# Kernel optimization log

Measured on AMD Instinct MI355X. Metric: run time of the kernel, lower is better.

## Reference

```python
import jax, jax.numpy as jnp
import numpy as np

DIM = 256
WIN = 7
HEADS = 8
HEAD_DIM = DIM // HEADS
N = WIN * WIN
NW = 64          # windows per image (56x56 map / 7x7 windows)
BATCH = 2048     # num_windows * image_batch (64 * 32)
SCALE = HEAD_DIM ** -0.5


def _relative_position_index(win_h, win_w):
    coords = np.stack(np.meshgrid(np.arange(win_h), np.arange(win_w), indexing='ij'))  # (2, h, w)
    flat = coords.reshape(2, -1)                     # (2, N)
    rel = flat[:, :, None] - flat[:, None, :]        # (2, N, N)
    rel = rel.transpose(1, 2, 0).astype(np.int32)    # (N, N, 2)
    rel[:, :, 0] += win_h - 1
    rel[:, :, 1] += win_w - 1
    rel[:, :, 0] *= 2 * win_w - 1
    return jnp.asarray(rel.sum(-1))                  # (N, N) int32


def setup_inputs() -> dict:
    key = jax.random.key(0)
    ks = jax.random.split(key, 6)
    x = jax.random.normal(ks[0], (BATCH, N, DIM), dtype=jnp.float32)
    mask = jnp.zeros((NW, N, N), dtype=jnp.float32)  # shift mask (0 / -inf); zeros = no shift
    qkv_w = jax.random.normal(ks[1], (3 * DIM, DIM), dtype=jnp.float32) * 0.02
    qkv_b = jnp.zeros((3 * DIM,), dtype=jnp.float32)
    bias_table = jax.random.normal(ks[2], ((2 * WIN - 1) ** 2, HEADS), dtype=jnp.float32) * 0.02
    proj_w = jax.random.normal(ks[3], (DIM, DIM), dtype=jnp.float32) * 0.02
    proj_b = jnp.zeros((DIM,), dtype=jnp.float32)
    rel_index = _relative_position_index(WIN, WIN)
    return {"x": x, "mask": mask, "qkv_w": qkv_w, "qkv_b": qkv_b,
            "bias_table": bias_table, "proj_w": proj_w, "proj_b": proj_b,
            "rel_index": rel_index}


def reference(x, mask, qkv_w, qkv_b, bias_table, proj_w, proj_b, rel_index):
    B, n, C = x.shape
    qkv = x @ qkv_w.T + qkv_b                                  # (B, N, 3C)
    qkv = qkv.reshape(B, n, 3, HEADS, HEAD_DIM)
    qkv = jnp.transpose(qkv, (2, 0, 3, 1, 4))                  # (3, B, H, N, hd)
    q, k, v = qkv[0], qkv[1], qkv[2]
    attn = jnp.einsum('bhnd,bhmd->bhnm', q * SCALE, k)         # (B, H, N, N)
    rel_bias = bias_table[rel_index.reshape(-1)].reshape(n, n, HEADS)
    attn = attn + jnp.transpose(rel_bias, (2, 0, 1))[None]     # + (1, H, N, N)
    nW = mask.shape[0]
    attn = attn.reshape(B // nW, nW, HEADS, n, n) + mask[None, :, None]
    attn = attn.reshape(B, HEADS, n, n)
    attn = jax.nn.softmax(attn, axis=-1)
    out = jnp.einsum('bhnm,bhmd->bhnd', attn, v)               # (B, H, N, hd)
    out = jnp.transpose(out, (0, 2, 1, 3)).reshape(B, n, C)
    return out @ proj_w.T + proj_b
```

## Files before the change

kernel.cpp:

```cpp
#include <hip/hip_runtime.h>

typedef float f32x4 __attribute__((ext_vector_type(4)));
typedef short s16x8 __attribute__((ext_vector_type(8)));
typedef unsigned int u32x4 __attribute__((ext_vector_type(4)));
typedef unsigned int u32x2 __attribute__((ext_vector_type(2)));
typedef __bf16 bf16x2 __attribute__((ext_vector_type(2)));
typedef unsigned short u16;
typedef unsigned int u32;

#define QK_SCALE 0.17677669529663687f
#define LOG2E    1.4426950408889634f
#define QK_SCALE_L2E 0.25504614517377436f

__device__ __forceinline__ u16 f2bf(float f) {
    __bf16 b = (__bf16)f;
    return __builtin_bit_cast(u16, b);
}
__device__ __forceinline__ u32 pk2(float lo, float hi) {
    bf16x2 v;
    v[0] = (__bf16)lo;
    v[1] = (__bf16)hi;
    return __builtin_bit_cast(u32, v);
}
__device__ __forceinline__ float swap32(float v, bool lt32) {
    u32 xi = __builtin_bit_cast(u32, v);
    u32x2 r = __builtin_amdgcn_permlane32_swap(xi, xi, false, false);
    return __builtin_bit_cast(float, lt32 ? r[1] : r[0]);
}
__device__ __forceinline__ float swap16(float v, bool lo16) {
    u32 xi = __builtin_bit_cast(u32, v);
    u32x2 r = __builtin_amdgcn_permlane16_swap(xi, xi, false, false);
    return __builtin_bit_cast(float, lo16 ? r[1] : r[0]);
}

__device__ __forceinline__ s16x8 frag4(u32 r0u0, u32 r1u0, u32 r0u1, u32 r1u1,
                                       int aA, int aB, bool lo) {
    u32x4 w;
    u32 a, bq;
    a  = (u32)__builtin_amdgcn_ds_bpermute(aA, (int)r0u0);
    bq = (u32)__builtin_amdgcn_ds_bpermute(aA, (int)r0u1);
    w[0] = lo ? a : bq;
    a  = (u32)__builtin_amdgcn_ds_bpermute(aA, (int)r1u0);
    bq = (u32)__builtin_amdgcn_ds_bpermute(aA, (int)r1u1);
    w[1] = lo ? a : bq;
    a  = (u32)__builtin_amdgcn_ds_bpermute(aB, (int)r0u0);
    bq = (u32)__builtin_amdgcn_ds_bpermute(aB, (int)r0u1);
    w[2] = lo ? a : bq;
    a  = (u32)__builtin_amdgcn_ds_bpermute(aB, (int)r1u0);
    bq = (u32)__builtin_amdgcn_ds_bpermute(aB, (int)r1u1);
    w[3] = lo ? a : bq;
    return __builtin_bit_cast(s16x8, w);
}

#define WS_PROJW 393216
#define WS_BMC   524288
#define WS_F32_NEED (524288 + 8388608)

__global__ void prep(const float* __restrict__ qkv_w, const float* __restrict__ proj_w,
                     const float* __restrict__ bias_table, const int* __restrict__ rel_index,
                     const float* __restrict__ mask,
                     u16* __restrict__ wqkvC2, u16* __restrict__ projwC,
                     u16* __restrict__ bmC2, float* __restrict__ bmF, int use_f32) {
    int i = blockIdx.x * 256 + threadIdx.x;
    if (i < 196608) {
        int e = i & 7, lane = (i >> 3) & 63, ks = (i >> 9) & 7, dt = (i >> 12) & 1;
        int i2 = i >> 13, t = i2 % 3, h = i2 / 3;
        int c = lane & 15, g = lane >> 4;
        wqkvC2[i] = f2bf(qkv_w[(t * 256 + h * 32 + dt * 16 + c) * 256 + ks * 32 + g * 8 + e]);
    }
    if (i < 65536) {
        int e = i & 7, lane = (i >> 3) & 63, ks = (i >> 9) & 7, nt = (i >> 12) & 15;
        int c = lane & 15, g = lane >> 4;
        projwC[i] = f2bf(proj_w[(nt * 16 + c) * 256 + ks * 32 + g * 8 + e]);
    }
    {
        int j = i & 3, lane = (i >> 2) & 63, mtK = (i >> 8) & 3, ntQ = (i >> 10) & 3;
        int h = (i >> 12) & 7, wi = i >> 15;
        int c = lane & 15, g = lane >> 4;
        int q = ntQ * 16 + c, k = mtK * 16 + g * 4 + j;
        float v;
        if (k < 49) v = (q < 49) ? bias_table[rel_index[q * 49 + k] * 8 + h]
                                   + mask[wi * 2401 + q * 49 + k]
                                 : 0.f;
        else        v = -1e30f;
        v *= LOG2E;
        if (use_f32) bmF[i] = v;
        else         bmC2[i] = f2bf(v);
    }
}

#define OUTSB 22152
template<bool F32BM>
__global__ __launch_bounds__(256, 2)
void swin_attn(const float* __restrict__ x,
               const float* __restrict__ qkv_b,
               const float* __restrict__ proj_b,
               const u16* __restrict__ wqkvC2,
               const u16* __restrict__ projwC,
               const u16* __restrict__ bmC2,
               const float* __restrict__ bmF,
               float* __restrict__ out) {
    __shared__ __align__(16) u16 sm[35088];
    const int b = blockIdx.x, tid = threadIdx.x;
    const int wv = tid >> 6, lane = tid & 63, g = lane >> 4, c = lane & 15;
    const int wi = b & 63;
    const int VTb = 12936 + wv * 2304;
    const float* xw = x + (size_t)b * 12544;

    for (int i = tid; i < 49 * 64; i += 256) {
        int row = i >> 6, q4 = i & 63;
        float4 v = ((const float4*)xw)[i];
        uint2 s;
        s.x = pk2(v.x, v.y);
        s.y = pk2(v.z, v.w);
        *(uint2*)&sm[row * 264 + q4 * 4] = s;
    }
    __syncthreads();

    const int addrA = ((lane & 15) + ((lane & 16) << 1)) << 2;
    const int addrB = addrA + 64;
    const bool lo = lane < 32;
    const bool l16 = (lane & 16) == 0;
    const s16x8 zfrag = {0, 0, 0, 0, 0, 0, 0, 0};

#pragma unroll
    for (int hl = 0; hl < 2; ++hl) {
        const int h = wv * 2 + hl;

        f32x4 acc[6][4];
#pragma unroll
        for (int f = 0; f < 6; ++f)
#pragma unroll
            for (int tt = 0; tt < 4; ++tt) acc[f][tt] = f32x4{0.f, 0.f, 0.f, 0.f};

        s16x8 wf[2][6];
#pragma unroll
        for (int f = 0; f < 6; ++f)
            wf[0][f] = *(const s16x8*)&wqkvC2[(((h * 6 + f) * 8 + 0) * 64 + lane) * 8];
        s16x8 Xf[2][4];
#pragma unroll
        for (int tt = 0; tt < 4; ++tt)
            Xf[0][tt] = *(const s16x8*)&sm[(tt * 16 + c) * 264 + g * 8];
        if (c > 0) Xf[0][3] = zfrag;
#pragma unroll
        for (int ks = 0; ks < 8; ++ks) {
            if (ks < 7) {
#pragma unroll
                for (int f = 0; f < 6; ++f)
                    wf[(ks + 1) & 1][f] =
                        *(const s16x8*)&wqkvC2[(((h * 6 + f) * 8 + (ks + 1)) * 64 + lane) * 8];
#pragma unroll
                for (int tt = 0; tt < 4; ++tt)
                    Xf[(ks + 1) & 1][tt] = *(const s16x8*)&sm[(tt * 16 + c) * 264 + (ks + 1) * 32 + g * 8];
                if (c > 0) Xf[(ks + 1) & 1][3] = zfrag;
            }
            __builtin_amdgcn_s_setprio(1);
#pragma unroll
            for (int f = 0; f < 6; ++f)
#pragma unroll
                for (int tt = 0; tt < 4; ++tt)
                    acc[f][tt] = __builtin_amdgcn_mfma_f32_16x16x32_bf16(wf[ks & 1][f], Xf[ks & 1][tt], acc[f][tt], 0, 0, 0);
            __builtin_amdgcn_s_setprio(0);
        }

        u32 qp[4][2][2], kp[4][2][2];
#pragma unroll
        for (int f = 0; f < 6; ++f) {
            int t = f >> 1, dt = f & 1;
            f32x4 bv = *(const f32x4*)&qkv_b[t * 256 + h * 32 + dt * 16 + g * 4];
#pragma unroll
            for (int tt = 0; tt < 4; ++tt) {
                float v0 = acc[f][tt][0] + bv[0];
                float v1 = acc[f][tt][1] + bv[1];
                float v2 = acc[f][tt][2] + bv[2];
                float v3 = acc[f][tt][3] + bv[3];
                if (t == 0) {
                    qp[tt][dt][0] = pk2(v0 * QK_SCALE_L2E, v1 * QK_SCALE_L2E);
                    qp[tt][dt][1] = pk2(v2 * QK_SCALE_L2E, v3 * QK_SCALE_L2E);
                } else if (t == 1) {
                    kp[tt][dt][0] = pk2(v0, v1);
                    kp[tt][dt][1] = pk2(v2, v3);
                } else {
                    sm[VTb + (dt * 16 + g * 4 + 0) * 72 + tt * 16 + c] = f2bf(v0);
                    sm[VTb + (dt * 16 + g * 4 + 1) * 72 + tt * 16 + c] = f2bf(v1);
                    sm[VTb + (dt * 16 + g * 4 + 2) * 72 + tt * 16 + c] = f2bf(v2);
                    sm[VTb + (dt * 16 + g * 4 + 3) * 72 + tt * 16 + c] = f2bf(v3);
                }
            }
        }

        f32x4 bmf[4][4];
        u32 bm0[4][4], bm1[4][4];
        if constexpr (F32BM) {
#pragma unroll
            for (int ntQ = 0; ntQ < 4; ++ntQ)
#pragma unroll
                for (int mtK = 0; mtK < 4; ++mtK)
                    bmf[ntQ][mtK] = *(const f32x4*)&bmF[((((wi * 8 + h) * 4 + ntQ) * 4 + mtK) * 64 + lane) * 4];
        } else {
#pragma unroll
            for (int ntQ = 0; ntQ < 4; ++ntQ)
#pragma unroll
                for (int mtK = 0; mtK < 4; ++mtK) {
                    const u32* bp = (const u32*)&bmC2[((((wi * 8 + h) * 4 + ntQ) * 4 + mtK) * 64 + lane) * 4];
                    bm0[ntQ][mtK] = bp[0];
                    bm1[ntQ][mtK] = bp[1];
                }
        }

        s16x8 Qf[4], Kf[4];
#pragma unroll
        for (int nt = 0; nt < 4; ++nt)
            Qf[nt] = frag4(qp[nt][0][0], qp[nt][0][1], qp[nt][1][0], qp[nt][1][1], addrA, addrB, lo);
#pragma unroll
        for (int mt = 0; mt < 4; ++mt)
            Kf[mt] = frag4(kp[mt][0][0], kp[mt][0][1], kp[mt][1][0], kp[mt][1][1], addrA, addrB, lo);

#pragma unroll
        for (int ntQ = 0; ntQ < 4; ++ntQ) {
            f32x4 lvc[4];
            __builtin_amdgcn_s_setprio(1);
#pragma unroll
            for (int mtK = 0; mtK < 4; ++mtK) {
                if constexpr (F32BM) {
                    lvc[mtK] = __builtin_amdgcn_mfma_f32_16x16x32_bf16(Kf[mtK], Qf[ntQ], bmf[ntQ][mtK], 0, 0, 0);
                } else {
                    f32x4 z = {0.f, 0.f, 0.f, 0.f};
                    lvc[mtK] = __builtin_amdgcn_mfma_f32_16x16x32_bf16(Kf[mtK], Qf[ntQ], z, 0, 0, 0);
                }
            }
            __builtin_amdgcn_s_setprio(0);
            float m = -1e30f;
#pragma unroll
            for (int mtK = 0; mtK < 3; ++mtK) {
                if constexpr (!F32BM) {
                    u32 w0 = bm0[ntQ][mtK], w1 = bm1[ntQ][mtK];
                    lvc[mtK][0] += __builtin_bit_cast(float, w0 << 16);
                    lvc[mtK][1] += __builtin_bit_cast(float, w0 & 0xffff0000u);
                    lvc[mtK][2] += __builtin_bit_cast(float, w1 << 16);
                    lvc[mtK][3] += __builtin_bit_cast(float, w1 & 0xffff0000u);
                }
                m = fmaxf(m, fmaxf(fmaxf(lvc[mtK][0], lvc[mtK][1]),
                                   fmaxf(lvc[mtK][2], lvc[mtK][3])));
            }
            if constexpr (!F32BM)
                lvc[3][0] += __builtin_bit_cast(float, bm0[ntQ][3] << 16);
            m = fmaxf(m, lvc[3][0]);
            m = fmaxf(m, swap16(m, l16));
            m = fmaxf(m, swap32(m, lo));
            float s = 0.f;
#pragma unroll
            for (int mtK = 0; mtK < 3; ++mtK)
#pragma unroll
                for (int j = 0; j < 4; ++j) {
                    float e = __builtin_amdgcn_exp2f(lvc[mtK][j] - m);
                    lvc[mtK][j] = e;
                    s += e;
                }
            float e3 = __builtin_amdgcn_exp2f(lvc[3][0] - m);
            lvc[3][0] = e3;
            s += e3;
            s += swap16(s, l16);
            s += swap32(s, lo);
            float is = __builtin_amdgcn_rcpf(s);
            u32 ppc[4][2];
#pragma unroll
            for (int mtK = 0; mtK < 3; ++mtK) {
                ppc[mtK][0] = pk2(lvc[mtK][0] * is, lvc[mtK][1] * is);
                ppc[mtK][1] = pk2(lvc[mtK][2] * is, lvc[mtK][3] * is);
            }
            ppc[3][0] = pk2(lvc[3][0] * is, 0.f);
            ppc[3][1] = 0;

            f32x4 o[2] = {{0.f, 0.f, 0.f, 0.f}, {0.f, 0.f, 0.f, 0.f}};
#pragma unroll
            for (int ks2 = 0; ks2 < 2; ++ks2) {
                s16x8 Pf = frag4(ppc[2 * ks2][0], ppc[2 * ks2][1],
                                 ppc[2 * ks2 + 1][0], ppc[2 * ks2 + 1][1], addrA, addrB, lo);
                s16x8 Vf0 = *(const s16x8*)&sm[VTb + (0 * 16 + c) * 72 + ks2 * 32 + g * 8];
                s16x8 Vf1 = *(const s16x8*)&sm[VTb + (1 * 16 + c) * 72 + ks2 * 32 + g * 8];
                __builtin_amdgcn_s_setprio(1);
                o[0] = __builtin_amdgcn_mfma_f32_16x16x32_bf16(Pf, Vf0, o[0], 0, 0, 0);
                o[1] = __builtin_amdgcn_mfma_f32_16x16x32_bf16(Pf, Vf1, o[1], 0, 0, 0);
                __builtin_amdgcn_s_setprio(0);
            }
#pragma unroll
            for (int ndt = 0; ndt < 2; ++ndt) {
                int colb = (wv * 2 + hl) * 32 + ndt * 16 + c;
                int row = ntQ * 16 + g * 4;
                if (row < 49)     sm[OUTSB + row * 264 + colb] = f2bf(o[ndt][0]);
                if (row + 1 < 49) sm[OUTSB + (row + 1) * 264 + colb] = f2bf(o[ndt][1]);
                if (row + 2 < 49) sm[OUTSB + (row + 2) * 264 + colb] = f2bf(o[ndt][2]);
                if (row + 3 < 49) sm[OUTSB + (row + 3) * 264 + colb] = f2bf(o[ndt][3]);
            }
        }
    }

    s16x8 pf[2][4];
#pragma unroll
    for (int n = 0; n < 4; ++n)
        pf[0][n] = *(const s16x8*)&projwC[(((wv * 4 + n) * 8 + 0) * 64 + lane) * 8];
    __syncthreads();

    f32x4 pacc[4][4];
#pragma unroll
    for (int mt = 0; mt < 4; ++mt)
#pragma unroll
        for (int n = 0; n < 4; ++n) pacc[mt][n] = f32x4{0.f, 0.f, 0.f, 0.f};
#pragma unroll
    for (int ks = 0; ks < 8; ++ks) {
        if (ks < 7) {
#pragma unroll
            for (int n = 0; n < 4; ++n)
                pf[(ks + 1) & 1][n] =
                    *(const s16x8*)&projwC[(((wv * 4 + n) * 8 + (ks + 1)) * 64 + lane) * 8];
        }
        s16x8 ao[4];
#pragma unroll
        for (int mt = 0; mt < 4; ++mt) {
            int row = mt * 16 + c; row = row > 48 ? 48 : row;
            ao[mt] = *(const s16x8*)&sm[OUTSB + row * 264 + ks * 32 + g * 8];
        }
        __builtin_amdgcn_s_setprio(1);
#pragma unroll
        for (int n = 0; n < 4; ++n)
#pragma unroll
            for (int mt = 0; mt < 4; ++mt)
                pacc[mt][n] = __builtin_amdgcn_mfma_f32_16x16x32_bf16(ao[mt], pf[ks & 1][n], pacc[mt][n], 0, 0, 0);
        __builtin_amdgcn_s_setprio(0);
    }
    float* ob = out + (size_t)b * 12544;
#pragma unroll
    for (int n = 0; n < 4; ++n) {
        int col = (wv * 4 + n) * 16 + c;
        float pb = proj_b[col];
#pragma unroll
        for (int mt = 0; mt < 4; ++mt)
#pragma unroll
            for (int j = 0; j < 4; ++j) {
                int row = mt * 16 + g * 4 + j;
                if (row < 49) ob[row * 256 + col] = pacc[mt][n][j] + pb;
            }
    }
}

extern "C" void kernel_launch(void* const* d_in, const int* in_sizes, int n_in,
                              void* d_out, int out_size, void* d_ws, size_t ws_size,
                              hipStream_t stream) {
    const float* x          = (const float*)d_in[0];
    const float* mask       = (const float*)d_in[1];
    const float* qkv_w      = (const float*)d_in[2];
    const float* qkv_b      = (const float*)d_in[3];
    const float* bias_table = (const float*)d_in[4];
    const float* proj_w     = (const float*)d_in[5];
    const float* proj_b     = (const float*)d_in[6];
    const int*   rel_index  = (const int*)d_in[7];

    u16*   wqkvC2 = (u16*)d_ws;
    u16*   projwC = (u16*)((char*)d_ws + WS_PROJW);
    u16*   bmC2   = (u16*)((char*)d_ws + WS_BMC);
    float* bmF    = (float*)((char*)d_ws + WS_BMC);

    const bool f32bm = ws_size >= (size_t)WS_F32_NEED;

    prep<<<8192, 256, 0, stream>>>(qkv_w, proj_w, bias_table, rel_index, mask,
                                   wqkvC2, projwC, bmC2, bmF, (int)f32bm);
    if (f32bm)
        swin_attn<true><<<2048, 256, 0, stream>>>(x, qkv_b, proj_b, wqkvC2, projwC,
                                                  bmC2, bmF, (float*)d_out);
    else
        swin_attn<false><<<2048, 256, 0, stream>>>(x, qkv_b, proj_b, wqkvC2, projwC,
                                                   bmC2, bmF, (float*)d_out);
}
```

Before: 106.8 us.

## Stage Q/K/P/V fragments through LDS instead of ds_bpermute shuffles

```diff
diff --git a/kernel.cpp b/kernel.cpp
--- a/kernel.cpp
+++ b/kernel.cpp
@@ -2,13 +2,11 @@
 
 typedef float f32x4 __attribute__((ext_vector_type(4)));
 typedef short s16x8 __attribute__((ext_vector_type(8)));
-typedef unsigned int u32x4 __attribute__((ext_vector_type(4)));
 typedef unsigned int u32x2 __attribute__((ext_vector_type(2)));
 typedef __bf16 bf16x2 __attribute__((ext_vector_type(2)));
 typedef unsigned short u16;
 typedef unsigned int u32;
 
-#define QK_SCALE 0.17677669529663687f
 #define LOG2E    1.4426950408889634f
 #define QK_SCALE_L2E 0.25504614517377436f
 
@@ -31,25 +29,6 @@
     u32 xi = __builtin_bit_cast(u32, v);
     u32x2 r = __builtin_amdgcn_permlane16_swap(xi, xi, false, false);
     return __builtin_bit_cast(float, lo16 ? r[1] : r[0]);
-}
-
-__device__ __forceinline__ s16x8 frag4(u32 r0u0, u32 r1u0, u32 r0u1, u32 r1u1,
-                                       int aA, int aB, bool lo) {
-    u32x4 w;
-    u32 a, bq;
-    a  = (u32)__builtin_amdgcn_ds_bpermute(aA, (int)r0u0);
-    bq = (u32)__builtin_amdgcn_ds_bpermute(aA, (int)r0u1);
-    w[0] = lo ? a : bq;
-    a  = (u32)__builtin_amdgcn_ds_bpermute(aA, (int)r1u0);
-    bq = (u32)__builtin_amdgcn_ds_bpermute(aA, (int)r1u1);
-    w[1] = lo ? a : bq;
-    a  = (u32)__builtin_amdgcn_ds_bpermute(aB, (int)r0u0);
-    bq = (u32)__builtin_amdgcn_ds_bpermute(aB, (int)r0u1);
-    w[2] = lo ? a : bq;
-    a  = (u32)__builtin_amdgcn_ds_bpermute(aB, (int)r1u0);
-    bq = (u32)__builtin_amdgcn_ds_bpermute(aB, (int)r1u1);
-    w[3] = lo ? a : bq;
-    return __builtin_bit_cast(s16x8, w);
 }
 
 #define WS_PROJW 393216
@@ -89,7 +68,6 @@
     }
 }
 
-#define OUTSB 22152
 template<bool F32BM>
 __global__ __launch_bounds__(256, 2)
 void swin_attn(const float* __restrict__ x,
@@ -100,29 +78,29 @@
                const u16* __restrict__ bmC2,
                const float* __restrict__ bmF,
                float* __restrict__ out) {
-    __shared__ __align__(16) u16 sm[35088];
+    __shared__ __align__(16) u16 sm[38152];
     const int b = blockIdx.x, tid = threadIdx.x;
     const int wv = tid >> 6, lane = tid & 63, g = lane >> 4, c = lane & 15;
     const int wi = b & 63;
-    const int VTb = 12936 + wv * 2304;
+    const int WB = 12936 + wv * 6304;
     const float* xw = x + (size_t)b * 12544;
 
     for (int i = tid; i < 49 * 64; i += 256) {
         int row = i >> 6, q4 = i & 63;
         float4 v = ((const float4*)xw)[i];
-        uint2 s;
-        s.x = pk2(v.x, v.y);
-        s.y = pk2(v.z, v.w);
-        *(uint2*)&sm[row * 264 + q4 * 4] = s;
+        u32x2 s;
+        s[0] = pk2(v.x, v.y);
+        s[1] = pk2(v.z, v.w);
+        *(u32x2*)&sm[row * 264 + q4 * 4] = s;
     }
     __syncthreads();
 
-    const int addrA = ((lane & 15) + ((lane & 16) << 1)) << 2;
-    const int addrB = addrA + 64;
     const bool lo = lane < 32;
     const bool l16 = (lane & 16) == 0;
     const s16x8 zfrag = {0, 0, 0, 0, 0, 0, 0, 0};
 
+    u32 opk[2][4][2][2];
+
 #pragma unroll
     for (int hl = 0; hl < 2; ++hl) {
         const int h = wv * 2 + hl;
@@ -158,72 +136,85 @@
 #pragma unroll
             for (int f = 0; f < 6; ++f)
 #pragma unroll
-                for (int tt = 0; tt < 4; ++tt)
-                    acc[f][tt] = __builtin_amdgcn_mfma_f32_16x16x32_bf16(wf[ks & 1][f], Xf[ks & 1][tt], acc[f][tt], 0, 0, 0);
+                for (int tt = 0; tt < 4; ++tt) {
+                    if (f < 4)
+                        acc[f][tt] = __builtin_amdgcn_mfma_f32_16x16x32_bf16(wf[ks & 1][f], Xf[ks & 1][tt], acc[f][tt], 0, 0, 0);
+                    else
+                        acc[f][tt] = __builtin_amdgcn_mfma_f32_16x16x32_bf16(Xf[ks & 1][tt], wf[ks & 1][f], acc[f][tt], 0, 0, 0);
+                }
             __builtin_amdgcn_s_setprio(0);
         }
 
-        u32 qp[4][2][2], kp[4][2][2];
 #pragma unroll
         for (int f = 0; f < 6; ++f) {
             int t = f >> 1, dt = f & 1;
-            f32x4 bv = *(const f32x4*)&qkv_b[t * 256 + h * 32 + dt * 16 + g * 4];
-#pragma unroll
-            for (int tt = 0; tt < 4; ++tt) {
-                float v0 = acc[f][tt][0] + bv[0];
-                float v1 = acc[f][tt][1] + bv[1];
-                float v2 = acc[f][tt][2] + bv[2];
-                float v3 = acc[f][tt][3] + bv[3];
-                if (t == 0) {
-                    qp[tt][dt][0] = pk2(v0 * QK_SCALE_L2E, v1 * QK_SCALE_L2E);
-                    qp[tt][dt][1] = pk2(v2 * QK_SCALE_L2E, v3 * QK_SCALE_L2E);
-                } else if (t == 1) {
-                    kp[tt][dt][0] = pk2(v0, v1);
-                    kp[tt][dt][1] = pk2(v2, v3);
-                } else {
-                    sm[VTb + (dt * 16 + g * 4 + 0) * 72 + tt * 16 + c] = f2bf(v0);
-                    sm[VTb + (dt * 16 + g * 4 + 1) * 72 + tt * 16 + c] = f2bf(v1);
-                    sm[VTb + (dt * 16 + g * 4 + 2) * 72 + tt * 16 + c] = f2bf(v2);
-                    sm[VTb + (dt * 16 + g * 4 + 3) * 72 + tt * 16 + c] = f2bf(v3);
-                }
-            }
-        }
-
-        f32x4 bmf[4][4];
-        u32 bm0[4][4], bm1[4][4];
-        if constexpr (F32BM) {
-#pragma unroll
-            for (int ntQ = 0; ntQ < 4; ++ntQ)
+            if (t < 2) {
+                f32x4 bv = *(const f32x4*)&qkv_b[t * 256 + h * 32 + dt * 16 + g * 4];
+                int base = (t == 0) ? WB : WB + 2000;
+#pragma unroll
+                for (int tt = 0; tt < 4; ++tt) {
+                    int row = tt * 16 + c;
+                    float v0 = acc[f][tt][0] + bv[0];
+                    float v1 = acc[f][tt][1] + bv[1];
+                    float v2 = acc[f][tt][2] + bv[2];
+                    float v3 = acc[f][tt][3] + bv[3];
+                    if (t == 0) {
+                        v0 *= QK_SCALE_L2E; v1 *= QK_SCALE_L2E;
+                        v2 *= QK_SCALE_L2E; v3 *= QK_SCALE_L2E;
+                    }
+                    if (row < 50) {
+                        u32x2 s;
+                        s[0] = pk2(v0, v1);
+                        s[1] = pk2(v2, v3);
+                        *(u32x2*)&sm[base + row * 40 + dt * 16 + g * 4] = s;
+                    }
+                }
+            } else {
+                float bvs = qkv_b[512 + h * 32 + dt * 16 + c];
+#pragma unroll
+                for (int tt = 0; tt < 4; ++tt) {
+                    u32x2 s;
+                    s[0] = pk2(acc[f][tt][0] + bvs, acc[f][tt][1] + bvs);
+                    s[1] = pk2(acc[f][tt][2] + bvs, acc[f][tt][3] + bvs);
+                    *(u32x2*)&sm[WB + 4000 + (dt * 16 + c) * 72 + tt * 16 + g * 4] = s;
+                }
+            }
+        }
+
+        s16x8 Qf[4], Kf[4];
+#pragma unroll
+        for (int nt = 0; nt < 4; ++nt) {
+            int row = nt * 16 + c; row = row > 49 ? 49 : row;
+            Qf[nt] = *(const s16x8*)&sm[WB + row * 40 + g * 8];
+        }
+#pragma unroll
+        for (int mt = 0; mt < 4; ++mt) {
+            int row = mt * 16 + c; row = row > 49 ? 49 : row;
+            Kf[mt] = *(const s16x8*)&sm[WB + 2000 + row * 40 + g * 8];
+        }
+
+#pragma unroll
+        for (int ntQ = 0; ntQ < 4; ++ntQ) {
+            f32x4 bmfc[4];
+            u32 bm0c[4], bm1c[4];
+            if constexpr (F32BM) {
 #pragma unroll
                 for (int mtK = 0; mtK < 4; ++mtK)
-                    bmf[ntQ][mtK] = *(const f32x4*)&bmF[((((wi * 8 + h) * 4 + ntQ) * 4 + mtK) * 64 + lane) * 4];
-        } else {
-#pragma unroll
-            for (int ntQ = 0; ntQ < 4; ++ntQ)
+                    bmfc[mtK] = *(const f32x4*)&bmF[((((wi * 8 + h) * 4 + ntQ) * 4 + mtK) * 64 + lane) * 4];
+            } else {
 #pragma unroll
                 for (int mtK = 0; mtK < 4; ++mtK) {
                     const u32* bp = (const u32*)&bmC2[((((wi * 8 + h) * 4 + ntQ) * 4 + mtK) * 64 + lane) * 4];
-                    bm0[ntQ][mtK] = bp[0];
-                    bm1[ntQ][mtK] = bp[1];
-                }
-        }
-
-        s16x8 Qf[4], Kf[4];
-#pragma unroll
-        for (int nt = 0; nt < 4; ++nt)
-            Qf[nt] = frag4(qp[nt][0][0], qp[nt][0][1], qp[nt][1][0], qp[nt][1][1], addrA, addrB, lo);
-#pragma unroll
-        for (int mt = 0; mt < 4; ++mt)
-            Kf[mt] = frag4(kp[mt][0][0], kp[mt][0][1], kp[mt][1][0], kp[mt][1][1], addrA, addrB, lo);
-
-#pragma unroll
-        for (int ntQ = 0; ntQ < 4; ++ntQ) {
+                    bm0c[mtK] = bp[0];
+                    bm1c[mtK] = bp[1];
+                }
+            }
             f32x4 lvc[4];
             __builtin_amdgcn_s_setprio(1);
 #pragma unroll
             for (int mtK = 0; mtK < 4; ++mtK) {
                 if constexpr (F32BM) {
-                    lvc[mtK] = __builtin_amdgcn_mfma_f32_16x16x32_bf16(Kf[mtK], Qf[ntQ], bmf[ntQ][mtK], 0, 0, 0);
+                    lvc[mtK] = __builtin_amdgcn_mfma_f32_16x16x32_bf16(Kf[mtK], Qf[ntQ], bmfc[mtK], 0, 0, 0);
                 } else {
                     f32x4 z = {0.f, 0.f, 0.f, 0.f};
                     lvc[mtK] = __builtin_amdgcn_mfma_f32_16x16x32_bf16(Kf[mtK], Qf[ntQ], z, 0, 0, 0);
@@ -234,7 +225,7 @@
 #pragma unroll
             for (int mtK = 0; mtK < 3; ++mtK) {
                 if constexpr (!F32BM) {
-                    u32 w0 = bm0[ntQ][mtK], w1 = bm1[ntQ][mtK];
+                    u32 w0 = bm0c[mtK], w1 = bm1c[mtK];
                     lvc[mtK][0] += __builtin_bit_cast(float, w0 << 16);
                     lvc[mtK][1] += __builtin_bit_cast(float, w0 & 0xffff0000u);
                     lvc[mtK][2] += __builtin_bit_cast(float, w1 << 16);
@@ -244,7 +235,7 @@
                                    fmaxf(lvc[mtK][2], lvc[mtK][3])));
             }
             if constexpr (!F32BM)
-                lvc[3][0] += __builtin_bit_cast(float, bm0[ntQ][3] << 16);
+                lvc[3][0] += __builtin_bit_cast(float, bm0c[3] << 16);
             m = fmaxf(m, lvc[3][0]);
             m = fmaxf(m, swap16(m, l16));
             m = fmaxf(m, swap32(m, lo));
@@ -258,27 +249,33 @@
                     s += e;
                 }
             float e3 = __builtin_amdgcn_exp2f(lvc[3][0] - m);
-            lvc[3][0] = e3;
             s += e3;
             s += swap16(s, l16);
             s += swap32(s, lo);
             float is = __builtin_amdgcn_rcpf(s);
-            u32 ppc[4][2];
-#pragma unroll
-            for (int mtK = 0; mtK < 3; ++mtK) {
-                ppc[mtK][0] = pk2(lvc[mtK][0] * is, lvc[mtK][1] * is);
-                ppc[mtK][1] = pk2(lvc[mtK][2] * is, lvc[mtK][3] * is);
-            }
-            ppc[3][0] = pk2(lvc[3][0] * is, 0.f);
-            ppc[3][1] = 0;
-
+
+            int q = ntQ * 16 + c;
+            if (q < 50) {
+#pragma unroll
+                for (int mtK = 0; mtK < 3; ++mtK) {
+                    u32x2 sP;
+                    sP[0] = pk2(lvc[mtK][0] * is, lvc[mtK][1] * is);
+                    sP[1] = pk2(lvc[mtK][2] * is, lvc[mtK][3] * is);
+                    *(u32x2*)&sm[WB + q * 72 + mtK * 16 + g * 4] = sP;
+                }
+                u32x2 sP3;
+                sP3[0] = pk2(e3 * is, 0.f);
+                sP3[1] = 0;
+                *(u32x2*)&sm[WB + q * 72 + 48 + g * 4] = sP3;
+            }
+
+            int prow = q > 49 ? 49 : q;
             f32x4 o[2] = {{0.f, 0.f, 0.f, 0.f}, {0.f, 0.f, 0.f, 0.f}};
 #pragma unroll
             for (int ks2 = 0; ks2 < 2; ++ks2) {
-                s16x8 Pf = frag4(ppc[2 * ks2][0], ppc[2 * ks2][1],
-                                 ppc[2 * ks2 + 1][0], ppc[2 * ks2 + 1][1], addrA, addrB, lo);
-                s16x8 Vf0 = *(const s16x8*)&sm[VTb + (0 * 16 + c) * 72 + ks2 * 32 + g * 8];
-                s16x8 Vf1 = *(const s16x8*)&sm[VTb + (1 * 16 + c) * 72 + ks2 * 32 + g * 8];
+                s16x8 Pf = *(const s16x8*)&sm[WB + prow * 72 + ks2 * 32 + g * 8];
+                s16x8 Vf0 = *(const s16x8*)&sm[WB + 4000 + c * 72 + ks2 * 32 + g * 8];
+                s16x8 Vf1 = *(const s16x8*)&sm[WB + 4000 + (16 + c) * 72 + ks2 * 32 + g * 8];
                 __builtin_amdgcn_s_setprio(1);
                 o[0] = __builtin_amdgcn_mfma_f32_16x16x32_bf16(Pf, Vf0, o[0], 0, 0, 0);
                 o[1] = __builtin_amdgcn_mfma_f32_16x16x32_bf16(Pf, Vf1, o[1], 0, 0, 0);
@@ -286,15 +283,27 @@
             }
 #pragma unroll
             for (int ndt = 0; ndt < 2; ++ndt) {
-                int colb = (wv * 2 + hl) * 32 + ndt * 16 + c;
-                int row = ntQ * 16 + g * 4;
-                if (row < 49)     sm[OUTSB + row * 264 + colb] = f2bf(o[ndt][0]);
-                if (row + 1 < 49) sm[OUTSB + (row + 1) * 264 + colb] = f2bf(o[ndt][1]);
-                if (row + 2 < 49) sm[OUTSB + (row + 2) * 264 + colb] = f2bf(o[ndt][2]);
-                if (row + 3 < 49) sm[OUTSB + (row + 3) * 264 + colb] = f2bf(o[ndt][3]);
-            }
-        }
-    }
+                opk[hl][ntQ][ndt][0] = pk2(o[ndt][0], o[ndt][1]);
+                opk[hl][ntQ][ndt][1] = pk2(o[ndt][2], o[ndt][3]);
+            }
+        }
+    }
+
+    __syncthreads();
+#pragma unroll
+    for (int hl = 0; hl < 2; ++hl)
+#pragma unroll
+        for (int mt = 0; mt < 4; ++mt)
+#pragma unroll
+            for (int n2 = 0; n2 < 2; ++n2)
+#pragma unroll
+                for (int jj = 0; jj < 2; ++jj) {
+                    u32 w = opk[hl][mt][n2][jj];
+                    int row = mt * 16 + g * 4 + jj * 2;
+                    int colb = (wv * 2 + hl) * 32 + n2 * 16 + c;
+                    if (row < 49)     sm[row * 264 + colb] = (u16)(w & 0xffffu);
+                    if (row + 1 < 49) sm[(row + 1) * 264 + colb] = (u16)(w >> 16);
+                }
 
     s16x8 pf[2][4];
 #pragma unroll
@@ -319,7 +328,7 @@
 #pragma unroll
         for (int mt = 0; mt < 4; ++mt) {
             int row = mt * 16 + c; row = row > 48 ? 48 : row;
-            ao[mt] = *(const s16x8*)&sm[OUTSB + row * 264 + ks * 32 + g * 8];
+            ao[mt] = *(const s16x8*)&sm[row * 264 + ks * 32 + g * 8];
         }
         __builtin_amdgcn_s_setprio(1);
 #pragma unroll
```

Result: slower. 109.0 us (+2.1%).
